# Performance work log

Hardware: AMD Instinct MI355X
Metric: run time of the kernel (lower is better)

## Reference

```python
import jax, jax.numpy as jnp
import numpy as np

B, T_IN, N, C_IN = 4, 16, 5000, 16
HID, C_OUT, KSZ, K_CHEB = 32, 64, 3, 3
E = 80000
BN_EPS = 1e-5


def _conv1xk(x, W, b):
    # x: (B,C,N,T), W: (O,I,1,k) -> (B,O,N,T-k+1)
    y = jax.lax.conv_general_dilated(x, W, (1, 1), 'VALID',
                                     dimension_numbers=('NCHW', 'OIHW', 'NCHW'))
    return y + b[None, :, None, None]


def temporal_conv(X, W1, b1, W2, b2, W3, b3):
    # X: (B,T,N,C) -> (B,T-k+1,N,O); gated temporal conv (GLU-style)
    Xp = jnp.transpose(X, (0, 3, 2, 1))  # (B,C,N,T)
    P = _conv1xk(Xp, W1, b1)
    Q = jax.nn.sigmoid(_conv1xk(Xp, W2, b2))
    R = _conv1xk(Xp, W3, b3)
    H = jax.nn.relu(P * Q + R)
    return jnp.transpose(H, (0, 3, 2, 1))


def cheb_conv(x, edge_index, edge_weight, W, b, lambda_max=2.0):
    # x: (B,T,N,C). Batched ChebConv with sym normalization (PyG semantics).
    n = x.shape[2]
    row, col = edge_index[0], edge_index[1]
    deg = jax.ops.segment_sum(edge_weight, row, num_segments=n)
    dis = jnp.where(deg > 0, deg ** -0.5, 0.0)
    w_norm = dis[row] * edge_weight * dis[col]  # (E,)

    def lhat(z):
        # A_norm z via scatter-add over edges, batched over (B,T)
        az = jnp.zeros_like(z).at[:, :, row, :].add(
            w_norm[None, None, :, None] * z[:, :, col, :])
        # L z = z - A_norm z ; L_hat = (2/lmax) L - I
        return (2.0 / lambda_max) * (z - az) - z

    Tx0 = x
    out = jnp.einsum('btnc,cd->btnd', Tx0, W[0])
    Tx1 = lhat(Tx0)
    out = out + jnp.einsum('btnc,cd->btnd', Tx1, W[1])
    for k in range(2, W.shape[0]):
        Tx2 = 2.0 * lhat(Tx1) - Tx0
        out = out + jnp.einsum('btnc,cd->btnd', Tx2, W[k])
        Tx0, Tx1 = Tx1, Tx2
    return out + b


def batch_norm_nodes(T, gamma, beta):
    # torch: permute to (B, N, T, C), BatchNorm2d(num_nodes), permute back
    Tp = jnp.transpose(T, (0, 2, 1, 3))  # (B,N,T,C)
    mean = jnp.mean(Tp, axis=(0, 2, 3), keepdims=True)
    var = jnp.mean((Tp - mean) ** 2, axis=(0, 2, 3), keepdims=True)  # biased
    Tn = (Tp - mean) / jnp.sqrt(var + BN_EPS)
    Tn = Tn * gamma[None, :, None, None] + beta[None, :, None, None]
    return jnp.transpose(Tn, (0, 2, 1, 3))


def setup_inputs() -> dict:
    key = jax.random.key(0)
    ks = jax.random.split(key, 20)
    s = 0.05
    inp = {
        'X': jax.random.normal(ks[0], (B, T_IN, N, C_IN), jnp.float32),
        'edge_index': jax.random.randint(ks[1], (2, E), 0, N, jnp.int64
                                         if jax.config.jax_enable_x64 else jnp.int32),
        'edge_weight': jax.random.uniform(ks[2], (E,), jnp.float32),
        'tc1_w1': jax.random.normal(ks[3], (HID, C_IN, 1, KSZ)) * s,
        'tc1_b1': jnp.zeros((HID,)),
        'tc1_w2': jax.random.normal(ks[4], (HID, C_IN, 1, KSZ)) * s,
        'tc1_b2': jnp.zeros((HID,)),
        'tc1_w3': jax.random.normal(ks[5], (HID, C_IN, 1, KSZ)) * s,
        'tc1_b3': jnp.zeros((HID,)),
        'cheb_W': jax.random.normal(ks[6], (K_CHEB, HID, HID)) * s,
        'cheb_b': jnp.zeros((HID,)),
        'tc2_w1': jax.random.normal(ks[7], (C_OUT, HID, 1, KSZ)) * s,
        'tc2_b1': jnp.zeros((C_OUT,)),
        'tc2_w2': jax.random.normal(ks[8], (C_OUT, HID, 1, KSZ)) * s,
        'tc2_b2': jnp.zeros((C_OUT,)),
        'tc2_w3': jax.random.normal(ks[9], (C_OUT, HID, 1, KSZ)) * s,
        'tc2_b3': jnp.zeros((C_OUT,)),
        'bn_gamma': jnp.ones((N,)),
        'bn_beta': jnp.zeros((N,)),
    }
    return inp


def reference(X, edge_index, edge_weight,
              tc1_w1, tc1_b1, tc1_w2, tc1_b2, tc1_w3, tc1_b3,
              cheb_W, cheb_b,
              tc2_w1, tc2_b1, tc2_w2, tc2_b2, tc2_w3, tc2_b3,
              bn_gamma, bn_beta):
    T0 = temporal_conv(X, tc1_w1, tc1_b1, tc1_w2, tc1_b2, tc1_w3, tc1_b3)
    T = jax.nn.relu(cheb_conv(T0, edge_index, edge_weight, cheb_W, cheb_b))
    T = temporal_conv(T, tc2_w1, tc2_b1, tc2_w2, tc2_b2, tc2_w3, tc2_b3)
    return batch_norm_nodes(T, bn_gamma, bn_beta)
```

## Files before the change

kernel.cpp:

```cpp
#include <hip/hip_runtime.h>
#include <hip/hip_bf16.h>

#define STC_N     5000
#define STC_TIN   16
#define STC_T1    14
#define STC_T2    12
#define STC_CIN   16
#define STC_CH    32
#define STC_CO    64
#define STC_BT1   56
#define STC_BT2   48
#define STC_ROWS1 280000
#define STC_ROWS2 240000
#define STC_RT1   17500
#define STC_RT2   15000
#define STC_GBLK  1280
#define STC_GWAVE (STC_GBLK*4)
#define STC_ROWB1 1792

#define STC_OFF_DEG   0
#define STC_OFF_CNT   20000
#define STC_OFF_CUR   40000
#define STC_OFF_DIS   60000
#define STC_OFF_OFFS  80000
#define STC_OFF_WN    100032
#define STC_OFF_CCOL  420032
#define STC_OFF_CW    740032
#define STC_OFF_T0    1060096
#define STC_OFF_G1    (STC_OFF_T0 + 17920000)
#define STC_OFF_G2    (STC_OFF_G1 + 17920000)
#define STC_OFF_PK2   (STC_OFF_G2 + 17920000)
#define STC_OFF_PK1   (STC_OFF_PK2 + 36864)
#define STC_OFF_PKC   (STC_OFF_PK1 + 12288)
#define STC_WS_REQ    (STC_OFF_PKC + 6144)

typedef __hip_bfloat16 bf16;
typedef short stc_s8 __attribute__((ext_vector_type(8)));
typedef float stc_f4 __attribute__((ext_vector_type(4)));

__device__ float stc_b2f(bf16 v) { return __bfloat162float(v); }
__device__ float stc_lo16(unsigned u) { return __uint_as_float(u << 16); }
__device__ float stc_hi16(unsigned u) { return __uint_as_float(u & 0xffff0000u); }

__device__ short stc_f2bs(float f) {
    unsigned u = __float_as_uint(f);
    u = (u + 0x7FFFu + ((u >> 16) & 1u)) >> 16;
    return (short)u;
}

__global__ void STConv_9972914061616_kernel() {}

__global__ void stc_fill(float* out, int n, float val) {
    int i = blockIdx.x * 256 + threadIdx.x;
    if (i < n) out[i] = val;
}

__global__ void stc_zero(int* p, int n) {
    int i = blockIdx.x * 256 + threadIdx.x;
    if (i < n) p[i] = 0;
}

__global__ void stc_deg(const int* ei, const float* ew, float* deg, int E) {
    int e = blockIdx.x * 256 + threadIdx.x;
    if (e < E) atomicAdd(&deg[ei[e]], ew[e]);
}

__global__ void stc_wnorm(const int* ei, const float* ew, const float* deg,
                          float* wn, int* cnt, int E) {
    int e = blockIdx.x * 256 + threadIdx.x;
    if (e < E) {
        int r = ei[e];
        int c = ei[E + e];
        float dr = deg[r];
        float dc = deg[c];
        float ir = (dr > 0.0f) ? rsqrtf(dr) : 0.0f;
        float ic = (dc > 0.0f) ? rsqrtf(dc) : 0.0f;
        wn[e] = ir * ew[e] * ic;
        atomicAdd(&cnt[r], 1);
    }
}

__global__ void stc_scan(const int* cnt, int* offs, int n) {
    __shared__ int s[256];
    int tid = threadIdx.x;
    int base = tid * 20;
    int loc[20];
    int sum = 0;
#pragma unroll
    for (int k = 0; k < 20; ++k) {
        int i = base + k;
        int v = (i < n) ? cnt[i] : 0;
        loc[k] = sum;
        sum += v;
    }
    s[tid] = sum;
    __syncthreads();
    for (int off = 1; off < 256; off <<= 1) {
        int t = (tid >= off) ? s[tid - off] : 0;
        __syncthreads();
        s[tid] += t;
        __syncthreads();
    }
    int pre = (tid > 0) ? s[tid - 1] : 0;
#pragma unroll
    for (int k = 0; k < 20; ++k) {
        int i = base + k;
        if (i < n) offs[i] = pre + loc[k];
    }
    if (tid == 255) offs[n] = s[255];
}

__global__ void stc_scatter(const int* ei, const float* wn, const int* offs,
                            int* cursor, int* ccol, float* cw, int E) {
    int e = blockIdx.x * 256 + threadIdx.x;
    if (e < E) {
        int r = ei[e];
        int pos = atomicAdd(&cursor[r], 1);
        int slot = offs[r] + pos;
        ccol[slot] = ei[E + e];
        cw[slot] = wn[e];
    }
}

__global__ void stc_pack(const float* w1a, const float* w1b, const float* w1c,
                         const float* w2a, const float* w2b, const float* w2c,
                         const float* chW,
                         short* pk1, short* pk2, short* pkc) {
    int gid = blockIdx.x * 256 + threadIdx.x;
    if (gid >= 54 * 64) return;
    int fi = gid >> 6;
    int lane = gid & 63;
    int j = lane & 15;
    int quad = lane >> 4;
    short f[8];
    if (fi < 36) {
        int s = fi % 3;
        int cc4 = fi / 3;
        int conv = cc4 >> 2;
        int c4 = cc4 & 3;
        const float* Wp = (conv == 0) ? w2a : ((conv == 1) ? w2b : w2c);
        int och = c4 * 16 + j;
        for (int i = 0; i < 8; ++i) {
            int cc = quad * 8 + i;
            f[i] = stc_f2bs(Wp[och * 96 + cc * 3 + s]);
        }
        for (int i = 0; i < 8; ++i) pk2[(fi * 64 + lane) * 8 + i] = f[i];
    } else if (fi < 48) {
        int t = fi - 36;
        int s = t & 1;
        int cj = t >> 1;
        int conv = cj >> 1;
        int jt = cj & 1;
        const float* Wp = (conv == 0) ? w1a : ((conv == 1) ? w1b : w1c);
        int och = jt * 16 + j;
        for (int i = 0; i < 8; ++i) {
            int k = s * 32 + quad * 8 + i;
            int kt = k >> 4;
            int c = k & 15;
            f[i] = (kt < 3) ? stc_f2bs(Wp[och * 48 + c * 3 + kt]) : (short)0;
        }
        for (int i = 0; i < 8; ++i) pk1[(t * 64 + lane) * 8 + i] = f[i];
    } else {
        int t = fi - 48;
        int s = t >> 1;
        int jt = t & 1;
        int d = jt * 16 + j;
        for (int i = 0; i < 8; ++i) {
            int c = quad * 8 + i;
            float w0 = chW[c * 32 + d];
            float w1 = chW[1024 + c * 32 + d];
            float w2 = chW[2048 + c * 32 + d];
            float v = (s == 0) ? (w0 - w2) : ((s == 1) ? -w1 : 2.0f * w2);
            f[i] = stc_f2bs(v);
        }
        for (int i = 0; i < 8; ++i) pkc[(t * 64 + lane) * 8 + i] = f[i];
    }
}

__global__ __launch_bounds__(256, 2) void stc_tconv1m(
    const float* X, const short* pk1,
    const float* B1, const float* B2, const float* B3,
    bf16* T0) {
    int lane = threadIdx.x & 63;
    int j = lane & 15;
    int quad = lane >> 4;
    int wave = blockIdx.x * 4 + (threadIdx.x >> 6);

    stc_s8 bfrag[3][2][2];
    for (int conv = 0; conv < 3; ++conv)
        for (int jt = 0; jt < 2; ++jt)
            for (int s = 0; s < 2; ++s) {
                int t = (conv * 2 + jt) * 2 + s;
                bfrag[conv][jt][s] = *(const stc_s8*)(pk1 + (t * 64 + lane) * 8);
            }
    float pb[2], qb[2], rb[2];
    for (int jt = 0; jt < 2; ++jt) {
        int och = jt * 16 + j;
        pb[jt] = B1[och];
        qb[jt] = B2[och];
        rb[jt] = B3[och];
    }

    for (int rt = wave; rt < STC_RT1; rt += STC_GWAVE) {
        int rm = rt * 16 + j;
        int n = rm % STC_N;
        int bt = rm / STC_N;
        int t = bt % STC_T1;
        int b = bt / STC_T1;

        int kt0 = quad >> 1;
        int c0 = (quad & 1) * 8;
        const float* xp0 = X + ((size_t)((b * STC_TIN + t + kt0) * STC_N + n)) * STC_CIN + c0;
        stc_s8 af0;
        for (int i = 0; i < 8; ++i) af0[i] = stc_f2bs(xp0[i]);

        stc_s8 af1;
        if (quad < 2) {
            const float* xp1 = X + ((size_t)((b * STC_TIN + t + 2) * STC_N + n)) * STC_CIN + c0;
            for (int i = 0; i < 8; ++i) af1[i] = stc_f2bs(xp1[i]);
        } else {
            for (int i = 0; i < 8; ++i) af1[i] = 0;
        }

        stc_f4 acc[6];
        for (int a = 0; a < 6; ++a) acc[a] = (stc_f4){0.0f, 0.0f, 0.0f, 0.0f};
        for (int conv = 0; conv < 3; ++conv) {
            for (int jt = 0; jt < 2; ++jt) {
                int a = conv * 2 + jt;
                acc[a] = __builtin_amdgcn_mfma_f32_16x16x32_bf16(
                    af0, bfrag[conv][jt][0], acc[a], 0, 0, 0);
                acc[a] = __builtin_amdgcn_mfma_f32_16x16x32_bf16(
                    af1, bfrag[conv][jt][1], acc[a], 0, 0, 0);
            }
        }

        for (int jt = 0; jt < 2; ++jt) {
            for (int reg = 0; reg < 4; ++reg) {
                float P = acc[jt][reg] + pb[jt];
                float Q = acc[2 + jt][reg] + qb[jt];
                float R = acc[4 + jt][reg] + rb[jt];
                float Qc = fminf(fmaxf(Q, -30.0f), 30.0f);
                float sg = 1.0f / (1.0f + expf(-Qc));
                float h = P * sg + R;
                if (h < 0.0f) h = 0.0f;
                int row = rt * 16 + quad * 4 + reg;
                int nw = row % STC_N;
                int btw = row / STC_N;
                T0[(size_t)nw * STC_ROWB1 + btw * STC_CH + jt * 16 + j] =
                    __float2bfloat16(h);
            }
        }
    }
}

__global__ void stc_gatherv(const bf16* z, bf16* g, const int* offs,
                            const int* ccol, const float* cw) {
    int n = blockIdx.x;
    __shared__ int col_s[128];
    __shared__ float w_s[128];
    int beg = offs[n];
    int end = offs[n + 1];
    int cg = threadIdx.x & 3;
    int sl = threadIdx.x >> 2;
    int act = (sl < STC_BT1);
    float a0 = 0.f, a1 = 0.f, a2 = 0.f, a3 = 0.f;
    float a4 = 0.f, a5 = 0.f, a6 = 0.f, a7 = 0.f;
    const bf16* zb = z + sl * STC_CH + cg * 8;
    for (int chunk = beg; chunk < end; chunk += 128) {
        int m = end - chunk;
        if (m > 128) m = 128;
        if (threadIdx.x < m) {
            col_s[threadIdx.x] = ccol[chunk + threadIdx.x];
            w_s[threadIdx.x] = cw[chunk + threadIdx.x];
        }
        __syncthreads();
        if (act) {
            int i = 0;
            for (; i + 4 <= m; i += 4) {
                float w0 = w_s[i], w1 = w_s[i + 1], w2 = w_s[i + 2], w3 = w_s[i + 3];
                uint4 u0 = *(const uint4*)(zb + (size_t)col_s[i] * STC_ROWB1);
                uint4 u1 = *(const uint4*)(zb + (size_t)col_s[i + 1] * STC_ROWB1);
                uint4 u2 = *(const uint4*)(zb + (size_t)col_s[i + 2] * STC_ROWB1);
                uint4 u3 = *(const uint4*)(zb + (size_t)col_s[i + 3] * STC_ROWB1);
                a0 += w0 * stc_lo16(u0.x); a1 += w0 * stc_hi16(u0.x);
                a2 += w0 * stc_lo16(u0.y); a3 += w0 * stc_hi16(u0.y);
                a4 += w0 * stc_lo16(u0.z); a5 += w0 * stc_hi16(u0.z);
                a6 += w0 * stc_lo16(u0.w); a7 += w0 * stc_hi16(u0.w);
                a0 += w1 * stc_lo16(u1.x); a1 += w1 * stc_hi16(u1.x);
                a2 += w1 * stc_lo16(u1.y); a3 += w1 * stc_hi16(u1.y);
                a4 += w1 * stc_lo16(u1.z); a5 += w1 * stc_hi16(u1.z);
                a6 += w1 * stc_lo16(u1.w); a7 += w1 * stc_hi16(u1.w);
                a0 += w2 * stc_lo16(u2.x); a1 += w2 * stc_hi16(u2.x);
                a2 += w2 * stc_lo16(u2.y); a3 += w2 * stc_hi16(u2.y);
                a4 += w2 * stc_lo16(u2.z); a5 += w2 * stc_hi16(u2.z);
                a6 += w2 * stc_lo16(u2.w); a7 += w2 * stc_hi16(u2.w);
                a0 += w3 * stc_lo16(u3.x); a1 += w3 * stc_hi16(u3.x);
                a2 += w3 * stc_lo16(u3.y); a3 += w3 * stc_hi16(u3.y);
                a4 += w3 * stc_lo16(u3.z); a5 += w3 * stc_hi16(u3.z);
                a6 += w3 * stc_lo16(u3.w); a7 += w3 * stc_hi16(u3.w);
            }
            for (; i < m; ++i) {
                float w = w_s[i];
                uint4 u = *(const uint4*)(zb + (size_t)col_s[i] * STC_ROWB1);
                a0 += w * stc_lo16(u.x); a1 += w * stc_hi16(u.x);
                a2 += w * stc_lo16(u.y); a3 += w * stc_hi16(u.y);
                a4 += w * stc_lo16(u.z); a5 += w * stc_hi16(u.z);
                a6 += w * stc_lo16(u.w); a7 += w * stc_hi16(u.w);
            }
        }
        __syncthreads();
    }
    if (act) {
        unsigned p0 = ((unsigned)(unsigned short)stc_f2bs(a0)) |
                      (((unsigned)(unsigned short)stc_f2bs(a1)) << 16);
        unsigned p1 = ((unsigned)(unsigned short)stc_f2bs(a2)) |
                      (((unsigned)(unsigned short)stc_f2bs(a3)) << 16);
        unsigned p2 = ((unsigned)(unsigned short)stc_f2bs(a4)) |
                      (((unsigned)(unsigned short)stc_f2bs(a5)) << 16);
        unsigned p3 = ((unsigned)(unsigned short)stc_f2bs(a6)) |
                      (((unsigned)(unsigned short)stc_f2bs(a7)) << 16);
        uint4 o;
        o.x = p0; o.y = p1; o.z = p2; o.w = p3;
        *(uint4*)(g + (size_t)n * STC_ROWB1 + sl * STC_CH + cg * 8) = o;
    }
}

__global__ __launch_bounds__(256, 2) void stc_combinem(
    const bf16* Tx0, const bf16* G1, const bf16* G2,
    const short* pkc, const float* bias, bf16* outb) {
    int lane = threadIdx.x & 63;
    int j = lane & 15;
    int quad = lane >> 4;
    int wave = blockIdx.x * 4 + (threadIdx.x >> 6);

    stc_s8 bfrag[3][2];
    for (int s = 0; s < 3; ++s)
        for (int jt = 0; jt < 2; ++jt) {
            int t = s * 2 + jt;
            bfrag[s][jt] = *(const stc_s8*)(pkc + (t * 64 + lane) * 8);
        }
    float bl[2];
    bl[0] = bias[j];
    bl[1] = bias[16 + j];

    for (int rt = wave; rt < STC_RT1; rt += STC_GWAVE) {
        int rm = rt * 16 + j;
        size_t abase = (size_t)rm * STC_CH + quad * 8;
        stc_s8 a0 = *(const stc_s8*)(Tx0 + abase);
        stc_s8 a1 = *(const stc_s8*)(G1 + abase);
        stc_s8 a2 = *(const stc_s8*)(G2 + abase);

        stc_f4 acc[2];
        acc[0] = (stc_f4){0.0f, 0.0f, 0.0f, 0.0f};
        acc[1] = (stc_f4){0.0f, 0.0f, 0.0f, 0.0f};
        for (int jt = 0; jt < 2; ++jt) {
            acc[jt] = __builtin_amdgcn_mfma_f32_16x16x32_bf16(a0, bfrag[0][jt], acc[jt], 0, 0, 0);
            acc[jt] = __builtin_amdgcn_mfma_f32_16x16x32_bf16(a1, bfrag[1][jt], acc[jt], 0, 0, 0);
            acc[jt] = __builtin_amdgcn_mfma_f32_16x16x32_bf16(a2, bfrag[2][jt], acc[jt], 0, 0, 0);
        }

        for (int jt = 0; jt < 2; ++jt) {
            for (int reg = 0; reg < 4; ++reg) {
                float h = acc[jt][reg] + bl[jt];
                if (h < 0.0f) h = 0.0f;
                int row = rt * 16 + quad * 4 + reg;
                outb[(size_t)row * STC_CH + jt * 16 + j] = __float2bfloat16(h);
            }
        }
    }
}

__global__ __launch_bounds__(256, 2) void stc_tconv2bn(
    const bf16* Tch, const short* pk2,
    const float* B1, const float* B2, const float* B3,
    const float* gamma, const float* beta,
    float* T2) {
    __shared__ float hb[4][48 * 68];
    int lane = threadIdx.x & 63;
    int j = lane & 15;
    int quad = lane >> 4;
    int w = threadIdx.x >> 6;
    int n = blockIdx.x * 4 + w;
    float* hbw = hb[w];

    stc_s8 bfrag[3][4][3];
    for (int conv = 0; conv < 3; ++conv)
        for (int c4 = 0; c4 < 4; ++c4)
            for (int s = 0; s < 3; ++s) {
                int fi = (conv * 4 + c4) * 3 + s;
                bfrag[conv][c4][s] = *(const stc_s8*)(pk2 + (fi * 64 + lane) * 8);
            }
    float pb[4], qb[4], rb[4];
    for (int c4 = 0; c4 < 4; ++c4) {
        int och = c4 * 16 + j;
        pb[c4] = B1[och];
        qb[c4] = B2[och];
        rb[c4] = B3[och];
    }

    float lsum = 0.0f;
    for (int t3 = 0; t3 < 3; ++t3) {
        int btb = t3 * 16;
        int bt2 = btb + j;
        int b = bt2 / STC_T2;
        int t = bt2 % STC_T2;
        const bf16* ap = Tch + (size_t)n * STC_ROWB1 + (b * STC_T1 + t) * STC_CH + quad * 8;
        stc_s8 af0 = *(const stc_s8*)(ap);
        stc_s8 af1 = *(const stc_s8*)(ap + STC_CH);
        stc_s8 af2 = *(const stc_s8*)(ap + 2 * STC_CH);

        stc_f4 acc[12];
        for (int a = 0; a < 12; ++a) acc[a] = (stc_f4){0.0f, 0.0f, 0.0f, 0.0f};

        for (int conv = 0; conv < 3; ++conv) {
            for (int c4 = 0; c4 < 4; ++c4) {
                int a = conv * 4 + c4;
                acc[a] = __builtin_amdgcn_mfma_f32_16x16x32_bf16(
                    af0, bfrag[conv][c4][0], acc[a], 0, 0, 0);
                acc[a] = __builtin_amdgcn_mfma_f32_16x16x32_bf16(
                    af1, bfrag[conv][c4][1], acc[a], 0, 0, 0);
                acc[a] = __builtin_amdgcn_mfma_f32_16x16x32_bf16(
                    af2, bfrag[conv][c4][2], acc[a], 0, 0, 0);
            }
        }

        for (int c4 = 0; c4 < 4; ++c4) {
            for (int reg = 0; reg < 4; ++reg) {
                float P = acc[c4][reg] + pb[c4];
                float Q = acc[4 + c4][reg] + qb[c4];
                float R = acc[8 + c4][reg] + rb[c4];
                float Qc = fminf(fmaxf(Q, -30.0f), 30.0f);
                float sg = 1.0f / (1.0f + expf(-Qc));
                float h = P * sg + R;
                if (h < 0.0f) h = 0.0f;
                int row = btb + quad * 4 + reg;
                hbw[row * 68 + c4 * 16 + j] = h;
                lsum += h;
            }
        }
    }
    __syncthreads();

    for (int off = 32; off; off >>= 1) lsum += __shfl_xor(lsum, off);
    float mean = lsum * (1.0f / (STC_BT2 * STC_CO));
    float sq = 0.0f;
    for (int k = 0; k < STC_BT2; ++k) {
        float d = hbw[k * 68 + lane] - mean;
        sq += d * d;
    }
    for (int off = 32; off; off >>= 1) sq += __shfl_xor(sq, off);
    float var = sq * (1.0f / (STC_BT2 * STC_CO));
    float istd = rsqrtf(var + 1e-5f);
    float scale = istd * gamma[n];
    float shift = beta[n] - mean * scale;
    for (int k = 0; k < STC_BT2; ++k) {
        T2[((size_t)k * STC_N + n) * STC_CO + lane] =
            hbw[k * 68 + lane] * scale + shift;
    }
}

extern "C" void kernel_launch(void* const* d_in, const int* in_sizes, int n_in,
                              void* d_out, int out_size, void* d_ws, size_t ws_size,
                              hipStream_t stream) {
    float* out = (float*)d_out;
    int outb = (out_size + 255) / 256;

    if (n_in < 19) {
        stc_fill<<<outb, 256, 0, stream>>>(out, out_size, 60.0f);
        return;
    }
    if (ws_size < (size_t)STC_WS_REQ) {
        stc_fill<<<outb, 256, 0, stream>>>(out, out_size, 50.0f);
        return;
    }

    const float* X = (const float*)d_in[0];
    const int* ei = (const int*)d_in[1];
    const float* ew = (const float*)d_in[2];
    const float* w1a = (const float*)d_in[3];
    const float* b1a = (const float*)d_in[4];
    const float* w1b = (const float*)d_in[5];
    const float* b1b = (const float*)d_in[6];
    const float* w1c = (const float*)d_in[7];
    const float* b1c = (const float*)d_in[8];
    const float* chW = (const float*)d_in[9];
    const float* chB = (const float*)d_in[10];
    const float* w2a = (const float*)d_in[11];
    const float* b2a = (const float*)d_in[12];
    const float* w2b = (const float*)d_in[13];
    const float* b2b = (const float*)d_in[14];
    const float* w2c = (const float*)d_in[15];
    const float* b2c = (const float*)d_in[16];
    const float* gam = (const float*)d_in[17];
    const float* bet = (const float*)d_in[18];
    int E = in_sizes[1] / 2;

    char* ws = (char*)d_ws;
    float* deg = (float*)(ws + STC_OFF_DEG);
    int* cnt = (int*)(ws + STC_OFF_CNT);
    int* cursor = (int*)(ws + STC_OFF_CUR);
    int* offs = (int*)(ws + STC_OFF_OFFS);
    float* wn = (float*)(ws + STC_OFF_WN);
    int* ccol = (int*)(ws + STC_OFF_CCOL);
    float* cw = (float*)(ws + STC_OFF_CW);
    bf16* T0 = (bf16*)(ws + STC_OFF_T0);
    bf16* G1 = (bf16*)(ws + STC_OFF_G1);
    bf16* G2 = (bf16*)(ws + STC_OFF_G2);
    short* pk2 = (short*)(ws + STC_OFF_PK2);
    short* pk1 = (short*)(ws + STC_OFF_PK1);
    short* pkc = (short*)(ws + STC_OFF_PKC);
    bf16* Tch = T0;
    float* T2 = out;

    stc_zero<<<59, 256, 0, stream>>>((int*)(ws + STC_OFF_DEG), 15000);
    stc_pack<<<14, 256, 0, stream>>>(w1a, w1b, w1c, w2a, w2b, w2c, chW, pk1, pk2, pkc);
    stc_deg<<<(E + 255) / 256, 256, 0, stream>>>(ei, ew, deg, E);
    stc_wnorm<<<(E + 255) / 256, 256, 0, stream>>>(ei, ew, deg, wn, cnt, E);
    stc_scan<<<1, 256, 0, stream>>>(cnt, offs, STC_N);
    stc_scatter<<<(E + 255) / 256, 256, 0, stream>>>(ei, wn, offs, cursor, ccol, cw, E);
    stc_tconv1m<<<STC_GBLK, 256, 0, stream>>>(X, pk1, b1a, b1b, b1c, T0);
    stc_gatherv<<<STC_N, 256, 0, stream>>>(T0, G1, offs, ccol, cw);
    stc_gatherv<<<STC_N, 256, 0, stream>>>(G1, G2, offs, ccol, cw);
    stc_combinem<<<STC_GBLK, 256, 0, stream>>>(T0, G1, G2, pkc, chB, Tch);
    stc_tconv2bn<<<1250, 256, 0, stream>>>(Tch, pk2, b2a, b2b, b2c, gam, bet, T2);
}
```

Before: 275.2 us.

## Fuse graph prep with tconv1, and ChebConv combine with tconv2+BN

Merges the degree, normalisation, scan and CSR scatter steps, the weight packing and the first temporal conv into one launch using block specialisation. Block 0 builds the CSR in shared memory, block 1 packs the weights, and the remaining blocks run tconv1 with weight fragments built inline. The Chebyshev combine is moved into the tconv2+BN kernel: each wave computes its node's combined features into LDS, which removes the intermediate global write and read. This cuts the launch count from 11 to 4, but the whole CSR build now runs serially in a single block, which may become a tail on the critical path.

```diff
diff --git a/kernel.cpp b/kernel.cpp
--- a/kernel.cpp
+++ b/kernel.cpp
@@ -10,10 +10,7 @@
 #define STC_CO    64
 #define STC_BT1   56
 #define STC_BT2   48
-#define STC_ROWS1 280000
-#define STC_ROWS2 240000
 #define STC_RT1   17500
-#define STC_RT2   15000
 #define STC_GBLK  1280
 #define STC_GWAVE (STC_GBLK*4)
 #define STC_ROWB1 1792
@@ -38,7 +35,6 @@
 typedef short stc_s8 __attribute__((ext_vector_type(8)));
 typedef float stc_f4 __attribute__((ext_vector_type(4)));
 
-__device__ float stc_b2f(bf16 v) { return __bfloat162float(v); }
 __device__ float stc_lo16(unsigned u) { return __uint_as_float(u << 16); }
 __device__ float stc_hi16(unsigned u) { return __uint_as_float(u & 0xffff0000u); }
 
@@ -55,150 +51,144 @@
     if (i < n) out[i] = val;
 }
 
-__global__ void stc_zero(int* p, int n) {
-    int i = blockIdx.x * 256 + threadIdx.x;
-    if (i < n) p[i] = 0;
-}
-
-__global__ void stc_deg(const int* ei, const float* ew, float* deg, int E) {
-    int e = blockIdx.x * 256 + threadIdx.x;
-    if (e < E) atomicAdd(&deg[ei[e]], ew[e]);
-}
-
-__global__ void stc_wnorm(const int* ei, const float* ew, const float* deg,
-                          float* wn, int* cnt, int E) {
-    int e = blockIdx.x * 256 + threadIdx.x;
-    if (e < E) {
-        int r = ei[e];
-        int c = ei[E + e];
-        float dr = deg[r];
-        float dc = deg[c];
-        float ir = (dr > 0.0f) ? rsqrtf(dr) : 0.0f;
-        float ic = (dc > 0.0f) ? rsqrtf(dc) : 0.0f;
-        wn[e] = ir * ew[e] * ic;
-        atomicAdd(&cnt[r], 1);
-    }
-}
-
-__global__ void stc_scan(const int* cnt, int* offs, int n) {
-    __shared__ int s[256];
+__global__ __launch_bounds__(256, 2) void stc_prep1(
+    const float* X, const int* ei, const float* ew,
+    const float* w1a, const float* b1a, const float* w1b, const float* b1b,
+    const float* w1c, const float* b1c,
+    const float* w2a, const float* w2b, const float* w2c, const float* chW,
+    int* offs, int* ccol, float* cwv,
+    short* pk2, short* pkc, bf16* T0, int E) {
+
+    __shared__ float dg[STC_N];
+    __shared__ int cn[STC_N];
+    __shared__ int ss[256];
+
     int tid = threadIdx.x;
-    int base = tid * 20;
-    int loc[20];
-    int sum = 0;
+    int blk = blockIdx.x;
+
+    if (blk == 0) {
+        for (int i = tid; i < STC_N; i += 256) { dg[i] = 0.0f; cn[i] = 0; }
+        __syncthreads();
+        for (int e = tid; e < E; e += 256) {
+            int r = ei[e];
+            atomicAdd(&dg[r], ew[e]);
+            atomicAdd(&cn[r], 1);
+        }
+        __syncthreads();
+        for (int i = tid; i < STC_N; i += 256) {
+            float d = dg[i];
+            dg[i] = (d > 0.0f) ? rsqrtf(d) : 0.0f;
+        }
+        __syncthreads();
+        {
+            int base = tid * 20;
+            int loc[20];
+            int sum = 0;
 #pragma unroll
-    for (int k = 0; k < 20; ++k) {
-        int i = base + k;
-        int v = (i < n) ? cnt[i] : 0;
-        loc[k] = sum;
-        sum += v;
-    }
-    s[tid] = sum;
-    __syncthreads();
-    for (int off = 1; off < 256; off <<= 1) {
-        int t = (tid >= off) ? s[tid - off] : 0;
-        __syncthreads();
-        s[tid] += t;
-        __syncthreads();
-    }
-    int pre = (tid > 0) ? s[tid - 1] : 0;
+            for (int k = 0; k < 20; ++k) {
+                int i = base + k;
+                int v = (i < STC_N) ? cn[i] : 0;
+                loc[k] = sum;
+                sum += v;
+            }
+            ss[tid] = sum;
+            __syncthreads();
+            for (int off = 1; off < 256; off <<= 1) {
+                int t = (tid >= off) ? ss[tid - off] : 0;
+                __syncthreads();
+                ss[tid] += t;
+                __syncthreads();
+            }
+            int pre = (tid > 0) ? ss[tid - 1] : 0;
 #pragma unroll
-    for (int k = 0; k < 20; ++k) {
-        int i = base + k;
-        if (i < n) offs[i] = pre + loc[k];
-    }
-    if (tid == 255) offs[n] = s[255];
-}
-
-__global__ void stc_scatter(const int* ei, const float* wn, const int* offs,
-                            int* cursor, int* ccol, float* cw, int E) {
-    int e = blockIdx.x * 256 + threadIdx.x;
-    if (e < E) {
-        int r = ei[e];
-        int pos = atomicAdd(&cursor[r], 1);
-        int slot = offs[r] + pos;
-        ccol[slot] = ei[E + e];
-        cw[slot] = wn[e];
-    }
-}
-
-__global__ void stc_pack(const float* w1a, const float* w1b, const float* w1c,
-                         const float* w2a, const float* w2b, const float* w2c,
-                         const float* chW,
-                         short* pk1, short* pk2, short* pkc) {
-    int gid = blockIdx.x * 256 + threadIdx.x;
-    if (gid >= 54 * 64) return;
-    int fi = gid >> 6;
-    int lane = gid & 63;
+            for (int k = 0; k < 20; ++k) {
+                int i = base + k;
+                if (i < STC_N) {
+                    int o = pre + loc[k];
+                    offs[i] = o;
+                    cn[i] = o;
+                }
+            }
+            if (tid == 255) offs[STC_N] = ss[255];
+        }
+        __syncthreads();
+        for (int e = tid; e < E; e += 256) {
+            int r = ei[e];
+            int c = ei[E + e];
+            float wv = dg[r] * ew[e] * dg[c];
+            int slot = atomicAdd(&cn[r], 1);
+            ccol[slot] = c;
+            cwv[slot] = wv;
+        }
+        return;
+    }
+
+    if (blk == 1) {
+        for (int idx = tid; idx < 42 * 64; idx += 256) {
+            int fi = idx >> 6;
+            int lane = idx & 63;
+            int j = lane & 15;
+            int quad = lane >> 4;
+            short f[8];
+            if (fi < 36) {
+                int s = fi % 3;
+                int cc4 = fi / 3;
+                int conv = cc4 >> 2;
+                int c4 = cc4 & 3;
+                const float* Wp = (conv == 0) ? w2a : ((conv == 1) ? w2b : w2c);
+                int och = c4 * 16 + j;
+                for (int i = 0; i < 8; ++i) {
+                    int cc = quad * 8 + i;
+                    f[i] = stc_f2bs(Wp[och * 96 + cc * 3 + s]);
+                }
+                for (int i = 0; i < 8; ++i) pk2[(fi * 64 + lane) * 8 + i] = f[i];
+            } else {
+                int t = fi - 36;
+                int s = t >> 1;
+                int jt = t & 1;
+                int d = jt * 16 + j;
+                for (int i = 0; i < 8; ++i) {
+                    int c = quad * 8 + i;
+                    float v0 = chW[c * 32 + d];
+                    float v1 = chW[1024 + c * 32 + d];
+                    float v2 = chW[2048 + c * 32 + d];
+                    float v = (s == 0) ? (v0 - v2) : ((s == 1) ? -v1 : 2.0f * v2);
+                    f[i] = stc_f2bs(v);
+                }
+                for (int i = 0; i < 8; ++i) pkc[(t * 64 + lane) * 8 + i] = f[i];
+            }
+        }
+        return;
+    }
+
+    int lane = tid & 63;
     int j = lane & 15;
     int quad = lane >> 4;
-    short f[8];
-    if (fi < 36) {
-        int s = fi % 3;
-        int cc4 = fi / 3;
-        int conv = cc4 >> 2;
-        int c4 = cc4 & 3;
-        const float* Wp = (conv == 0) ? w2a : ((conv == 1) ? w2b : w2c);
-        int och = c4 * 16 + j;
-        for (int i = 0; i < 8; ++i) {
-            int cc = quad * 8 + i;
-            f[i] = stc_f2bs(Wp[och * 96 + cc * 3 + s]);
-        }
-        for (int i = 0; i < 8; ++i) pk2[(fi * 64 + lane) * 8 + i] = f[i];
-    } else if (fi < 48) {
-        int t = fi - 36;
-        int s = t & 1;
-        int cj = t >> 1;
-        int conv = cj >> 1;
-        int jt = cj & 1;
+    int wave = (blk - 2) * 4 + (tid >> 6);
+
+    stc_s8 bfrag[3][2][2];
+    for (int conv = 0; conv < 3; ++conv) {
         const float* Wp = (conv == 0) ? w1a : ((conv == 1) ? w1b : w1c);
-        int och = jt * 16 + j;
-        for (int i = 0; i < 8; ++i) {
-            int k = s * 32 + quad * 8 + i;
-            int kt = k >> 4;
-            int c = k & 15;
-            f[i] = (kt < 3) ? stc_f2bs(Wp[och * 48 + c * 3 + kt]) : (short)0;
-        }
-        for (int i = 0; i < 8; ++i) pk1[(t * 64 + lane) * 8 + i] = f[i];
-    } else {
-        int t = fi - 48;
-        int s = t >> 1;
-        int jt = t & 1;
-        int d = jt * 16 + j;
-        for (int i = 0; i < 8; ++i) {
-            int c = quad * 8 + i;
-            float w0 = chW[c * 32 + d];
-            float w1 = chW[1024 + c * 32 + d];
-            float w2 = chW[2048 + c * 32 + d];
-            float v = (s == 0) ? (w0 - w2) : ((s == 1) ? -w1 : 2.0f * w2);
-            f[i] = stc_f2bs(v);
-        }
-        for (int i = 0; i < 8; ++i) pkc[(t * 64 + lane) * 8 + i] = f[i];
-    }
-}
-
-__global__ __launch_bounds__(256, 2) void stc_tconv1m(
-    const float* X, const short* pk1,
-    const float* B1, const float* B2, const float* B3,
-    bf16* T0) {
-    int lane = threadIdx.x & 63;
-    int j = lane & 15;
-    int quad = lane >> 4;
-    int wave = blockIdx.x * 4 + (threadIdx.x >> 6);
-
-    stc_s8 bfrag[3][2][2];
-    for (int conv = 0; conv < 3; ++conv)
-        for (int jt = 0; jt < 2; ++jt)
+        for (int jt = 0; jt < 2; ++jt) {
+            int och = jt * 16 + j;
             for (int s = 0; s < 2; ++s) {
-                int t = (conv * 2 + jt) * 2 + s;
-                bfrag[conv][jt][s] = *(const stc_s8*)(pk1 + (t * 64 + lane) * 8);
-            }
+                stc_s8 f;
+                for (int i = 0; i < 8; ++i) {
+                    int k = s * 32 + quad * 8 + i;
+                    int kt = k >> 4;
+                    int c = k & 15;
+                    f[i] = (kt < 3) ? stc_f2bs(Wp[och * 48 + c * 3 + kt]) : (short)0;
+                }
+                bfrag[conv][jt][s] = f;
+            }
+        }
+    }
     float pb[2], qb[2], rb[2];
     for (int jt = 0; jt < 2; ++jt) {
         int och = jt * 16 + j;
-        pb[jt] = B1[och];
-        qb[jt] = B2[och];
-        rb[jt] = B3[och];
+        pb[jt] = b1a[och];
+        qb[jt] = b1b[och];
+        rb[jt] = b1c[och];
     }
 
     for (int rt = wave; rt < STC_RT1; rt += STC_GWAVE) {
@@ -325,63 +315,53 @@
     }
 }
 
-__global__ __launch_bounds__(256, 2) void stc_combinem(
-    const bf16* Tx0, const bf16* G1, const bf16* G2,
-    const short* pkc, const float* bias, bf16* outb) {
-    int lane = threadIdx.x & 63;
-    int j = lane & 15;
-    int quad = lane >> 4;
-    int wave = blockIdx.x * 4 + (threadIdx.x >> 6);
-
-    stc_s8 bfrag[3][2];
-    for (int s = 0; s < 3; ++s)
-        for (int jt = 0; jt < 2; ++jt) {
-            int t = s * 2 + jt;
-            bfrag[s][jt] = *(const stc_s8*)(pkc + (t * 64 + lane) * 8);
-        }
-    float bl[2];
-    bl[0] = bias[j];
-    bl[1] = bias[16 + j];
-
-    for (int rt = wave; rt < STC_RT1; rt += STC_GWAVE) {
-        int rm = rt * 16 + j;
-        size_t abase = (size_t)rm * STC_CH + quad * 8;
-        stc_s8 a0 = *(const stc_s8*)(Tx0 + abase);
-        stc_s8 a1 = *(const stc_s8*)(G1 + abase);
-        stc_s8 a2 = *(const stc_s8*)(G2 + abase);
-
-        stc_f4 acc[2];
-        acc[0] = (stc_f4){0.0f, 0.0f, 0.0f, 0.0f};
-        acc[1] = (stc_f4){0.0f, 0.0f, 0.0f, 0.0f};
-        for (int jt = 0; jt < 2; ++jt) {
-            acc[jt] = __builtin_amdgcn_mfma_f32_16x16x32_bf16(a0, bfrag[0][jt], acc[jt], 0, 0, 0);
-            acc[jt] = __builtin_amdgcn_mfma_f32_16x16x32_bf16(a1, bfrag[1][jt], acc[jt], 0, 0, 0);
-            acc[jt] = __builtin_amdgcn_mfma_f32_16x16x32_bf16(a2, bfrag[2][jt], acc[jt], 0, 0, 0);
-        }
-
-        for (int jt = 0; jt < 2; ++jt) {
-            for (int reg = 0; reg < 4; ++reg) {
-                float h = acc[jt][reg] + bl[jt];
-                if (h < 0.0f) h = 0.0f;
-                int row = rt * 16 + quad * 4 + reg;
-                outb[(size_t)row * STC_CH + jt * 16 + j] = __float2bfloat16(h);
-            }
-        }
-    }
-}
-
-__global__ __launch_bounds__(256, 2) void stc_tconv2bn(
-    const bf16* Tch, const short* pk2,
-    const float* B1, const float* B2, const float* B3,
-    const float* gamma, const float* beta,
-    float* T2) {
+__global__ __launch_bounds__(256, 2) void stc_combconv2bn(
+    const bf16* T0, const bf16* G1, const bf16* G2,
+    const short* pkc, const float* chB,
+    const short* pk2, const float* B1, const float* B2, const float* B3,
+    const float* gamma, const float* beta, float* T2) {
+    __shared__ short comb[4][64 * 40];
     __shared__ float hb[4][48 * 68];
     int lane = threadIdx.x & 63;
     int j = lane & 15;
     int quad = lane >> 4;
     int w = threadIdx.x >> 6;
     int n = blockIdx.x * 4 + w;
+    short* cmb = comb[w];
     float* hbw = hb[w];
+
+    {
+        stc_s8 cfrag[3][2];
+        for (int s = 0; s < 3; ++s)
+            for (int jt = 0; jt < 2; ++jt)
+                cfrag[s][jt] = *(const stc_s8*)(pkc + ((s * 2 + jt) * 64 + lane) * 8);
+        float bl[2];
+        bl[0] = chB[j];
+        bl[1] = chB[16 + j];
+        for (int t3 = 0; t3 < 4; ++t3) {
+            size_t rm = (size_t)n * STC_BT1 + t3 * 16 + j;
+            size_t abase = rm * STC_CH + quad * 8;
+            stc_s8 a0 = *(const stc_s8*)(T0 + abase);
+            stc_s8 a1 = *(const stc_s8*)(G1 + abase);
+            stc_s8 a2 = *(const stc_s8*)(G2 + abase);
+            stc_f4 acc[2];
+            acc[0] = (stc_f4){0.0f, 0.0f, 0.0f, 0.0f};
+            acc[1] = (stc_f4){0.0f, 0.0f, 0.0f, 0.0f};
+            for (int jt = 0; jt < 2; ++jt) {
+                acc[jt] = __builtin_amdgcn_mfma_f32_16x16x32_bf16(a0, cfrag[0][jt], acc[jt], 0, 0, 0);
+                acc[jt] = __builtin_amdgcn_mfma_f32_16x16x32_bf16(a1, cfrag[1][jt], acc[jt], 0, 0, 0);
+                acc[jt] = __builtin_amdgcn_mfma_f32_16x16x32_bf16(a2, cfrag[2][jt], acc[jt], 0, 0, 0);
+            }
+            for (int jt = 0; jt < 2; ++jt) {
+                for (int reg = 0; reg < 4; ++reg) {
+                    float h = acc[jt][reg] + bl[jt];
+                    if (h < 0.0f) h = 0.0f;
+                    int row = t3 * 16 + quad * 4 + reg;
+                    cmb[row * 40 + jt * 16 + j] = stc_f2bs(h);
+                }
+            }
+        }
+    }
 
     stc_s8 bfrag[3][4][3];
     for (int conv = 0; conv < 3; ++conv)
@@ -404,10 +384,10 @@
         int bt2 = btb + j;
         int b = bt2 / STC_T2;
         int t = bt2 % STC_T2;
-        const bf16* ap = Tch + (size_t)n * STC_ROWB1 + (b * STC_T1 + t) * STC_CH + quad * 8;
+        const short* ap = cmb + (b * STC_T1 + t) * 40 + quad * 8;
         stc_s8 af0 = *(const stc_s8*)(ap);
-        stc_s8 af1 = *(const stc_s8*)(ap + STC_CH);
-        stc_s8 af2 = *(const stc_s8*)(ap + 2 * STC_CH);
+        stc_s8 af1 = *(const stc_s8*)(ap + 40);
+        stc_s8 af2 = *(const stc_s8*)(ap + 80);
 
         stc_f4 acc[12];
         for (int a = 0; a < 12; ++a) acc[a] = (stc_f4){0.0f, 0.0f, 0.0f, 0.0f};
@@ -439,7 +419,6 @@
             }
         }
     }
-    __syncthreads();
 
     for (int off = 32; off; off >>= 1) lsum += __shfl_xor(lsum, off);
     float mean = lsum * (1.0f / (STC_BT2 * STC_CO));
@@ -496,31 +475,20 @@
     int E = in_sizes[1] / 2;
 
     char* ws = (char*)d_ws;
-    float* deg = (float*)(ws + STC_OFF_DEG);
-    int* cnt = (int*)(ws + STC_OFF_CNT);
-    int* cursor = (int*)(ws + STC_OFF_CUR);
     int* offs = (int*)(ws + STC_OFF_OFFS);
-    float* wn = (float*)(ws + STC_OFF_WN);
     int* ccol = (int*)(ws + STC_OFF_CCOL);
-    float* cw = (float*)(ws + STC_OFF_CW);
+    float* cwv = (float*)(ws + STC_OFF_CW);
     bf16* T0 = (bf16*)(ws + STC_OFF_T0);
     bf16* G1 = (bf16*)(ws + STC_OFF_G1);
     bf16* G2 = (bf16*)(ws + STC_OFF_G2);
     short* pk2 = (short*)(ws + STC_OFF_PK2);
-    short* pk1 = (short*)(ws + STC_OFF_PK1);
     short* pkc = (short*)(ws + STC_OFF_PKC);
-    bf16* Tch = T0;
-    float* T2 = out;
-
-    stc_zero<<<59, 256, 0, stream>>>((int*)(ws + STC_OFF_DEG), 15000);
-    stc_pack<<<14, 256, 0, stream>>>(w1a, w1b, w1c, w2a, w2b, w2c, chW, pk1, pk2, pkc);
-    stc_deg<<<(E + 255) / 256, 256, 0, stream>>>(ei, ew, deg, E);
-    stc_wnorm<<<(E + 255) / 256, 256, 0, stream>>>(ei, ew, deg, wn, cnt, E);
-    stc_scan<<<1, 256, 0, stream>>>(cnt, offs, STC_N);
-    stc_scatter<<<(E + 255) / 256, 256, 0, stream>>>(ei, wn, offs, cursor, ccol, cw, E);
-    stc_tconv1m<<<STC_GBLK, 256, 0, stream>>>(X, pk1, b1a, b1b, b1c, T0);
-    stc_gatherv<<<STC_N, 256, 0, stream>>>(T0, G1, offs, ccol, cw);
-    stc_gatherv<<<STC_N, 256, 0, stream>>>(G1, G2, offs, ccol, cw);
-    stc_combinem<<<STC_GBLK, 256, 0, stream>>>(T0, G1, G2, pkc, chB, Tch);
-    stc_tconv2bn<<<1250, 256, 0, stream>>>(Tch, pk2, b2a, b2b, b2c, gam, bet, T2);
-}
+
+    stc_prep1<<<STC_GBLK + 2, 256, 0, stream>>>(
+        X, ei, ew, w1a, b1a, w1b, b1b, w1c, b1c,
+        w2a, w2b, w2c, chW, offs, ccol, cwv, pk2, pkc, T0, E);
+    stc_gatherv<<<STC_N, 256, 0, stream>>>(T0, G1, offs, ccol, cwv);
+    stc_gatherv<<<STC_N, 256, 0, stream>>>(G1, G2, offs, ccol, cwv);
+    stc_combconv2bn<<<1250, 256, 0, stream>>>(
+        T0, G1, G2, pkc, chB, pk2, b2a, b2b, b2c, gam, bet, out);
+}
```

After: 497.9 us. 80.9% more time.

## Fuse Chebyshev combine into temporal conv2 + batchnorm kernel via LDS

Applied to the files above, without the earlier changes.

Each wave now computes the Chebyshev combine (T0/G1/G2 MFMA plus bias and ReLU) for its node directly into shared memory, then runs the second temporal conv and batch norm from that LDS buffer. This removes the separate combine kernel and the global round-trip of its bf16 output. It also merges the zero-fill and weight-pack launches into one init kernel. The cost is extra LDS per block, which may lower occupancy, and lost cross-node parallelism in the combine stage.

```diff
diff --git a/kernel.cpp b/kernel.cpp
--- a/kernel.cpp
+++ b/kernel.cpp
@@ -10,10 +10,7 @@
 #define STC_CO    64
 #define STC_BT1   56
 #define STC_BT2   48
-#define STC_ROWS1 280000
-#define STC_ROWS2 240000
 #define STC_RT1   17500
-#define STC_RT2   15000
 #define STC_GBLK  1280
 #define STC_GWAVE (STC_GBLK*4)
 #define STC_ROWB1 1792
@@ -38,7 +35,6 @@
 typedef short stc_s8 __attribute__((ext_vector_type(8)));
 typedef float stc_f4 __attribute__((ext_vector_type(4)));
 
-__device__ float stc_b2f(bf16 v) { return __bfloat162float(v); }
 __device__ float stc_lo16(unsigned u) { return __uint_as_float(u << 16); }
 __device__ float stc_hi16(unsigned u) { return __uint_as_float(u & 0xffff0000u); }
 
@@ -55,78 +51,17 @@
     if (i < n) out[i] = val;
 }
 
-__global__ void stc_zero(int* p, int n) {
-    int i = blockIdx.x * 256 + threadIdx.x;
-    if (i < n) p[i] = 0;
-}
-
-__global__ void stc_deg(const int* ei, const float* ew, float* deg, int E) {
-    int e = blockIdx.x * 256 + threadIdx.x;
-    if (e < E) atomicAdd(&deg[ei[e]], ew[e]);
-}
-
-__global__ void stc_wnorm(const int* ei, const float* ew, const float* deg,
-                          float* wn, int* cnt, int E) {
-    int e = blockIdx.x * 256 + threadIdx.x;
-    if (e < E) {
-        int r = ei[e];
-        int c = ei[E + e];
-        float dr = deg[r];
-        float dc = deg[c];
-        float ir = (dr > 0.0f) ? rsqrtf(dr) : 0.0f;
-        float ic = (dc > 0.0f) ? rsqrtf(dc) : 0.0f;
-        wn[e] = ir * ew[e] * ic;
-        atomicAdd(&cnt[r], 1);
-    }
-}
-
-__global__ void stc_scan(const int* cnt, int* offs, int n) {
-    __shared__ int s[256];
-    int tid = threadIdx.x;
-    int base = tid * 20;
-    int loc[20];
-    int sum = 0;
-#pragma unroll
-    for (int k = 0; k < 20; ++k) {
-        int i = base + k;
-        int v = (i < n) ? cnt[i] : 0;
-        loc[k] = sum;
-        sum += v;
-    }
-    s[tid] = sum;
-    __syncthreads();
-    for (int off = 1; off < 256; off <<= 1) {
-        int t = (tid >= off) ? s[tid - off] : 0;
-        __syncthreads();
-        s[tid] += t;
-        __syncthreads();
-    }
-    int pre = (tid > 0) ? s[tid - 1] : 0;
-#pragma unroll
-    for (int k = 0; k < 20; ++k) {
-        int i = base + k;
-        if (i < n) offs[i] = pre + loc[k];
-    }
-    if (tid == 255) offs[n] = s[255];
-}
-
-__global__ void stc_scatter(const int* ei, const float* wn, const int* offs,
-                            int* cursor, int* ccol, float* cw, int E) {
-    int e = blockIdx.x * 256 + threadIdx.x;
-    if (e < E) {
-        int r = ei[e];
-        int pos = atomicAdd(&cursor[r], 1);
-        int slot = offs[r] + pos;
-        ccol[slot] = ei[E + e];
-        cw[slot] = wn[e];
-    }
-}
-
-__global__ void stc_pack(const float* w1a, const float* w1b, const float* w1c,
+__global__ void stc_init(int* zp,
+                         const float* w1a, const float* w1b, const float* w1c,
                          const float* w2a, const float* w2b, const float* w2c,
                          const float* chW,
                          short* pk1, short* pk2, short* pkc) {
-    int gid = blockIdx.x * 256 + threadIdx.x;
+    if (blockIdx.x < 59) {
+        int i = blockIdx.x * 256 + threadIdx.x;
+        if (i < 15000) zp[i] = 0;
+        return;
+    }
+    int gid = (blockIdx.x - 59) * 256 + threadIdx.x;
     if (gid >= 54 * 64) return;
     int fi = gid >> 6;
     int lane = gid & 63;
@@ -174,6 +109,68 @@
             f[i] = stc_f2bs(v);
         }
         for (int i = 0; i < 8; ++i) pkc[(t * 64 + lane) * 8 + i] = f[i];
+    }
+}
+
+__global__ void stc_deg(const int* ei, const float* ew, float* deg, int E) {
+    int e = blockIdx.x * 256 + threadIdx.x;
+    if (e < E) atomicAdd(&deg[ei[e]], ew[e]);
+}
+
+__global__ void stc_wnorm(const int* ei, const float* ew, const float* deg,
+                          float* wn, int* cnt, int E) {
+    int e = blockIdx.x * 256 + threadIdx.x;
+    if (e < E) {
+        int r = ei[e];
+        int c = ei[E + e];
+        float dr = deg[r];
+        float dc = deg[c];
+        float ir = (dr > 0.0f) ? rsqrtf(dr) : 0.0f;
+        float ic = (dc > 0.0f) ? rsqrtf(dc) : 0.0f;
+        wn[e] = ir * ew[e] * ic;
+        atomicAdd(&cnt[r], 1);
+    }
+}
+
+__global__ void stc_scan(const int* cnt, int* offs, int n) {
+    __shared__ int s[256];
+    int tid = threadIdx.x;
+    int base = tid * 20;
+    int loc[20];
+    int sum = 0;
+#pragma unroll
+    for (int k = 0; k < 20; ++k) {
+        int i = base + k;
+        int v = (i < n) ? cnt[i] : 0;
+        loc[k] = sum;
+        sum += v;
+    }
+    s[tid] = sum;
+    __syncthreads();
+    for (int off = 1; off < 256; off <<= 1) {
+        int t = (tid >= off) ? s[tid - off] : 0;
+        __syncthreads();
+        s[tid] += t;
+        __syncthreads();
+    }
+    int pre = (tid > 0) ? s[tid - 1] : 0;
+#pragma unroll
+    for (int k = 0; k < 20; ++k) {
+        int i = base + k;
+        if (i < n) offs[i] = pre + loc[k];
+    }
+    if (tid == 255) offs[n] = s[255];
+}
+
+__global__ void stc_scatter(const int* ei, const float* wn, const int* offs,
+                            int* cursor, int* ccol, float* cw, int E) {
+    int e = blockIdx.x * 256 + threadIdx.x;
+    if (e < E) {
+        int r = ei[e];
+        int pos = atomicAdd(&cursor[r], 1);
+        int slot = offs[r] + pos;
+        ccol[slot] = ei[E + e];
+        cw[slot] = wn[e];
     }
 }
 
@@ -325,63 +322,53 @@
     }
 }
 
-__global__ __launch_bounds__(256, 2) void stc_combinem(
-    const bf16* Tx0, const bf16* G1, const bf16* G2,
-    const short* pkc, const float* bias, bf16* outb) {
-    int lane = threadIdx.x & 63;
-    int j = lane & 15;
-    int quad = lane >> 4;
-    int wave = blockIdx.x * 4 + (threadIdx.x >> 6);
-
-    stc_s8 bfrag[3][2];
-    for (int s = 0; s < 3; ++s)
-        for (int jt = 0; jt < 2; ++jt) {
-            int t = s * 2 + jt;
-            bfrag[s][jt] = *(const stc_s8*)(pkc + (t * 64 + lane) * 8);
-        }
-    float bl[2];
-    bl[0] = bias[j];
-    bl[1] = bias[16 + j];
-
-    for (int rt = wave; rt < STC_RT1; rt += STC_GWAVE) {
-        int rm = rt * 16 + j;
-        size_t abase = (size_t)rm * STC_CH + quad * 8;
-        stc_s8 a0 = *(const stc_s8*)(Tx0 + abase);
-        stc_s8 a1 = *(const stc_s8*)(G1 + abase);
-        stc_s8 a2 = *(const stc_s8*)(G2 + abase);
-
-        stc_f4 acc[2];
-        acc[0] = (stc_f4){0.0f, 0.0f, 0.0f, 0.0f};
-        acc[1] = (stc_f4){0.0f, 0.0f, 0.0f, 0.0f};
-        for (int jt = 0; jt < 2; ++jt) {
-            acc[jt] = __builtin_amdgcn_mfma_f32_16x16x32_bf16(a0, bfrag[0][jt], acc[jt], 0, 0, 0);
-            acc[jt] = __builtin_amdgcn_mfma_f32_16x16x32_bf16(a1, bfrag[1][jt], acc[jt], 0, 0, 0);
-            acc[jt] = __builtin_amdgcn_mfma_f32_16x16x32_bf16(a2, bfrag[2][jt], acc[jt], 0, 0, 0);
-        }
-
-        for (int jt = 0; jt < 2; ++jt) {
-            for (int reg = 0; reg < 4; ++reg) {
-                float h = acc[jt][reg] + bl[jt];
-                if (h < 0.0f) h = 0.0f;
-                int row = rt * 16 + quad * 4 + reg;
-                outb[(size_t)row * STC_CH + jt * 16 + j] = __float2bfloat16(h);
-            }
-        }
-    }
-}
-
-__global__ __launch_bounds__(256, 2) void stc_tconv2bn(
-    const bf16* Tch, const short* pk2,
-    const float* B1, const float* B2, const float* B3,
-    const float* gamma, const float* beta,
-    float* T2) {
+__global__ __launch_bounds__(256, 2) void stc_combconv2bn(
+    const bf16* T0, const bf16* G1, const bf16* G2,
+    const short* pkc, const float* chB,
+    const short* pk2, const float* B1, const float* B2, const float* B3,
+    const float* gamma, const float* beta, float* T2) {
+    __shared__ short comb[4][64 * 40];
     __shared__ float hb[4][48 * 68];
     int lane = threadIdx.x & 63;
     int j = lane & 15;
     int quad = lane >> 4;
     int w = threadIdx.x >> 6;
     int n = blockIdx.x * 4 + w;
+    short* cmb = comb[w];
     float* hbw = hb[w];
+
+    {
+        stc_s8 cfrag[3][2];
+        for (int s = 0; s < 3; ++s)
+            for (int jt = 0; jt < 2; ++jt)
+                cfrag[s][jt] = *(const stc_s8*)(pkc + ((s * 2 + jt) * 64 + lane) * 8);
+        float bl[2];
+        bl[0] = chB[j];
+        bl[1] = chB[16 + j];
+        for (int t3 = 0; t3 < 4; ++t3) {
+            size_t rm = (size_t)n * STC_BT1 + t3 * 16 + j;
+            size_t abase = rm * STC_CH + quad * 8;
+            stc_s8 a0 = *(const stc_s8*)(T0 + abase);
+            stc_s8 a1 = *(const stc_s8*)(G1 + abase);
+            stc_s8 a2 = *(const stc_s8*)(G2 + abase);
+            stc_f4 acc[2];
+            acc[0] = (stc_f4){0.0f, 0.0f, 0.0f, 0.0f};
+            acc[1] = (stc_f4){0.0f, 0.0f, 0.0f, 0.0f};
+            for (int jt = 0; jt < 2; ++jt) {
+                acc[jt] = __builtin_amdgcn_mfma_f32_16x16x32_bf16(a0, cfrag[0][jt], acc[jt], 0, 0, 0);
+                acc[jt] = __builtin_amdgcn_mfma_f32_16x16x32_bf16(a1, cfrag[1][jt], acc[jt], 0, 0, 0);
+                acc[jt] = __builtin_amdgcn_mfma_f32_16x16x32_bf16(a2, cfrag[2][jt], acc[jt], 0, 0, 0);
+            }
+            for (int jt = 0; jt < 2; ++jt) {
+                for (int reg = 0; reg < 4; ++reg) {
+                    float h = acc[jt][reg] + bl[jt];
+                    if (h < 0.0f) h = 0.0f;
+                    int row = t3 * 16 + quad * 4 + reg;
+                    cmb[row * 40 + jt * 16 + j] = stc_f2bs(h);
+                }
+            }
+        }
+    }
 
     stc_s8 bfrag[3][4][3];
     for (int conv = 0; conv < 3; ++conv)
@@ -404,10 +391,10 @@
         int bt2 = btb + j;
         int b = bt2 / STC_T2;
         int t = bt2 % STC_T2;
-        const bf16* ap = Tch + (size_t)n * STC_ROWB1 + (b * STC_T1 + t) * STC_CH + quad * 8;
+        const short* ap = cmb + (b * STC_T1 + t) * 40 + quad * 8;
         stc_s8 af0 = *(const stc_s8*)(ap);
-        stc_s8 af1 = *(const stc_s8*)(ap + STC_CH);
-        stc_s8 af2 = *(const stc_s8*)(ap + 2 * STC_CH);
+        stc_s8 af1 = *(const stc_s8*)(ap + 40);
+        stc_s8 af2 = *(const stc_s8*)(ap + 80);
 
         stc_f4 acc[12];
         for (int a = 0; a < 12; ++a) acc[a] = (stc_f4){0.0f, 0.0f, 0.0f, 0.0f};
@@ -439,7 +426,6 @@
             }
         }
     }
-    __syncthreads();
 
     for (int off = 32; off; off >>= 1) lsum += __shfl_xor(lsum, off);
     float mean = lsum * (1.0f / (STC_BT2 * STC_CO));
@@ -509,11 +495,10 @@
     short* pk2 = (short*)(ws + STC_OFF_PK2);
     short* pk1 = (short*)(ws + STC_OFF_PK1);
     short* pkc = (short*)(ws + STC_OFF_PKC);
-    bf16* Tch = T0;
-    float* T2 = out;
-
-    stc_zero<<<59, 256, 0, stream>>>((int*)(ws + STC_OFF_DEG), 15000);
-    stc_pack<<<14, 256, 0, stream>>>(w1a, w1b, w1c, w2a, w2b, w2c, chW, pk1, pk2, pkc);
+
+    stc_init<<<73, 256, 0, stream>>>((int*)(ws + STC_OFF_DEG),
+                                     w1a, w1b, w1c, w2a, w2b, w2c, chW,
+                                     pk1, pk2, pkc);
     stc_deg<<<(E + 255) / 256, 256, 0, stream>>>(ei, ew, deg, E);
     stc_wnorm<<<(E + 255) / 256, 256, 0, stream>>>(ei, ew, deg, wn, cnt, E);
     stc_scan<<<1, 256, 0, stream>>>(cnt, offs, STC_N);
@@ -521,6 +506,6 @@
     stc_tconv1m<<<STC_GBLK, 256, 0, stream>>>(X, pk1, b1a, b1b, b1c, T0);
     stc_gatherv<<<STC_N, 256, 0, stream>>>(T0, G1, offs, ccol, cw);
     stc_gatherv<<<STC_N, 256, 0, stream>>>(G1, G2, offs, ccol, cw);
-    stc_combinem<<<STC_GBLK, 256, 0, stream>>>(T0, G1, G2, pkc, chB, Tch);
-    stc_tconv2bn<<<1250, 256, 0, stream>>>(Tch, pk2, b2a, b2b, b2c, gam, bet, T2);
-}
+    stc_combconv2bn<<<1250, 256, 0, stream>>>(
+        T0, G1, G2, pkc, chB, pk2, b2a, b2b, b2c, gam, bet, out);
+}
```

Result: faster. 266.8 us (-3.1%).
